# Kernel tuning notes

Measured on AMD Instinct MI355X. Metric: run time of the kernel, lower is better.

Reference implementation:

```python
import jax, jax.numpy as jnp
import numpy as np

B, N, D = 32, 1024, 128


def setup_inputs() -> dict:
    key = jax.random.key(0)
    ks = jax.random.split(key, 8)
    scale = 0.05
    P = jax.random.normal(ks[0], (B, N, D), dtype=jnp.float32)
    w_itr_att = jax.random.normal(ks[1], (3 * D,), dtype=jnp.float32) * scale
    w1 = jax.random.normal(ks[2], (2 * D, D), dtype=jnp.float32) * scale
    w2 = jax.random.normal(ks[3], (2 * D, D), dtype=jnp.float32) * scale
    w3 = jax.random.normal(ks[4], (2 * D, D), dtype=jnp.float32) * scale
    b1 = jnp.zeros((D,), dtype=jnp.float32)
    b2 = jnp.zeros((D,), dtype=jnp.float32)
    b3 = jnp.zeros((D,), dtype=jnp.float32)
    return {"P": P, "w_itr_att": w_itr_att, "w1": w1, "w2": w2,
            "w3": w3, "b1": b1, "b2": b2, "b3": b3}


def reference(P, w_itr_att, w1, w2, w3, b1, b2, b3):
    # P: [b, n, d]
    d = P.shape[-1]
    # Original builds alphaP[b,i,:,j] = concat(P[b,j], P[b,i], P[b,j]*P[b,i])
    # and A[b,i,j] = w_itr_att . alphaP[b,i,:,j]. Decompose w to avoid the
    # O(n^2 * 3d) tensor while computing identical math.
    wa, wb, wc = w_itr_att[:d], w_itr_att[d:2 * d], w_itr_att[2 * d:]
    A = (P @ wb)[:, :, None] + (P @ wa)[:, None, :] \
        + jnp.einsum('bid,bjd->bij', P * wc, P)  # [b, n, n]
    SA = jax.nn.softmax(A, axis=-1)              # softmax over j (axis=2)
    itr_attn = jnp.einsum('bij,bjd->bid', SA, P)  # batch_dot(SA, P)
    # Fuse gate (dropout is identity at inference)
    P_concat = jnp.concatenate([P, itr_attn], axis=2)  # [b, n, 2d]
    z = jnp.tanh(P_concat @ w1 + b1)
    r = jax.nn.sigmoid(P_concat @ w2 + b2)
    f = jax.nn.sigmoid(P_concat @ w3 + b3)
    return r * P + f * z
```

## Files before the change

### kernel.cpp

```cpp
#include <hip/hip_runtime.h>
#include <math.h>

#define BB 32
#define NN 1024
#define DD 128

typedef __bf16 bf16;
typedef bf16 bf16x4 __attribute__((ext_vector_type(4)));
typedef bf16 bf16x8 __attribute__((ext_vector_type(8)));
typedef float f32x4 __attribute__((ext_vector_type(4)));
typedef float f32x16 __attribute__((ext_vector_type(16)));

#define MFMA16(a, b, c) __builtin_amdgcn_mfma_f32_16x16x32_bf16(a, b, c, 0, 0, 0)
#define MFMA32(a, b, c) __builtin_amdgcn_mfma_f32_32x32x16_bf16(a, b, c, 0, 0, 0)

__device__ inline bf16x4 swap32(bf16x4 v) {
    union { bf16x4 h; int i[2]; } u, r;
    u.h = v;
    r.i[0] = __shfl_xor(u.i[0], 32, 64);
    r.i[1] = __shfl_xor(u.i[1], 32, 64);
    return r.h;
}

#define LTS 133
__global__ __launch_bounds__(256) void k_prep(const float* __restrict__ P,
                                              const float* __restrict__ w_itr,
                                              bf16* __restrict__ Xbf,
                                              bf16* __restrict__ Pq,
                                              bf16* __restrict__ Ptp,
                                              float* __restrict__ t) {
    __shared__ float Lt[64 * LTS];
    int tid = threadIdx.x;
    int b = blockIdx.x >> 4, g = blockIdx.x & 15;
    int n0 = g * 64;
    long base = ((long)b * NN + n0) * DD;
#pragma unroll
    for (int i = 0; i < 8; ++i) {
        int idx = tid + i * 256;
        int row = idx >> 5, c4 = idx & 31;
        *(float4*)&Lt[row * LTS + c4 * 4] = *(const float4*)&P[base + row * 128 + c4 * 4];
    }
    __syncthreads();
    {
        int row = tid >> 2, q = tid & 3;
        float s = 0.f;
#pragma unroll
        for (int kk = 0; kk < 32; ++kk) {
            int k = 4 * kk + q;
            s += Lt[row * LTS + k] * w_itr[k];
        }
        s += __shfl_xor(s, 1);
        s += __shfl_xor(s, 2);
        if (q == 0) t[(long)b * NN + n0 + row] = s;
    }
    const float* wc = w_itr + 2 * DD;
#pragma unroll
    for (int i = 0; i < 4; ++i) {
        int idx = tid + i * 256;
        int row = idx >> 4, seg = idx & 15;
        float4 va = *(const float4*)&Lt[row * LTS + seg * 8];
        float4 vb = *(const float4*)&Lt[row * LTS + seg * 8 + 4];
        float4 wa4 = *(const float4*)&wc[seg * 8];
        float4 wb4 = *(const float4*)&wc[seg * 8 + 4];
        float fv[8] = {va.x, va.y, va.z, va.w, vb.x, vb.y, vb.z, vb.w};
        float wv[8] = {wa4.x, wa4.y, wa4.z, wa4.w, wb4.x, wb4.y, wb4.z, wb4.w};
        bf16x8 xv, qv;
#pragma unroll
        for (int e = 0; e < 8; ++e) {
            xv[e] = (bf16)fv[e];
            qv[e] = (bf16)(fv[e] * wv[e]);
        }
        long rowg = (long)b * NN + n0 + row;
        *(bf16x8*)&Xbf[rowg * 128 + seg * 8] = xv;
        *(bf16x8*)&Pq[rowg * 128 + seg * 8] = qv;
    }
#pragma unroll
    for (int i = 0; i < 4; ++i) {
        int idx = tid + i * 256;
        int d = idx >> 3, c = idx & 7;
        bf16x8 v;
#pragma unroll
        for (int e = 0; e < 8; ++e) v[e] = (bf16)Lt[(c * 8 + e) * LTS + d];
        *(bf16x8*)&Ptp[((long)b * DD + d) * NN + n0 + c * 8] = v;
    }
}

__global__ __launch_bounds__(256) void k_prepw(const float* __restrict__ w1,
                                               const float* __restrict__ w2,
                                               const float* __restrict__ w3,
                                               bf16* __restrict__ WtG) {
    __shared__ float Lw[32][33];
    int bi = blockIdx.x;
    int mat = bi >> 5, rem = bi & 31;
    int kt = rem >> 2, ct = rem & 3;
    const float* wsrc = (mat == 0) ? w1 : ((mat == 1) ? w2 : w3);
    int tid = threadIdx.x;
#pragma unroll
    for (int p = 0; p < 4; ++p) {
        int idx = tid + p * 256;
        int kr = idx >> 5, c = idx & 31;
        Lw[kr][c] = wsrc[(kt * 32 + kr) * DD + ct * 32 + c];
    }
    __syncthreads();
    int colg = tid >> 3, kq = tid & 7;
    bf16x4 v;
#pragma unroll
    for (int e = 0; e < 4; ++e) v[e] = (bf16)Lw[kq * 4 + e][colg];
    *(bf16x4*)&WtG[(mat * 128 + ct * 32 + colg) * 256 + kt * 32 + kq * 4] = v;
}

__global__ __launch_bounds__(256, 3) void k_attn(const bf16* __restrict__ Xbf,
                                                 const bf16* __restrict__ Pq,
                                                 const bf16* __restrict__ Ptp,
                                                 const float* __restrict__ t,
                                                 const bf16* __restrict__ WtG,
                                                 const float* __restrict__ b1,
                                                 const float* __restrict__ b2,
                                                 const float* __restrict__ b3,
                                                 float* __restrict__ out) {
    __shared__ __align__(16) char smem[51200];
    float* PA   = (float*)smem;
    bf16*  Wst  = (bf16*)smem;
    float* ost  = (float*)smem;
    bf16*  Xsh  = (bf16*)(smem + 33792);
    float* lbuf = (float*)(smem + 50688);

    const int tid = threadIdx.x;
    const int kh = tid >> 6, lane = tid & 63;
    const int col = lane & 31, q = lane >> 5;
    const int b = blockIdx.x & 31, qt = blockIdx.x >> 5;
    const long qrow0 = (long)b * NN + qt * 32;
    const long kvrow = (long)b * NN;

    bf16x8 Qb[8];
#pragma unroll
    for (int c = 0; c < 8; ++c)
        Qb[c] = *(const bf16x8*)&Pq[(qrow0 + col) * 128 + c * 16 + q * 8];

    f32x16 O[4];
#pragma unroll
    for (int mt = 0; mt < 4; ++mt)
#pragma unroll
        for (int r = 0; r < 16; ++r) O[mt][r] = 0.f;
    float lsum = 0.f;

    for (int kt = 0; kt < 8; ++kt) {
        int j0 = kh * 256 + kt * 32;
        bf16x8 kf[8];
#pragma unroll
        for (int c = 0; c < 8; ++c)
            kf[c] = *(const bf16x8*)&Xbf[(kvrow + j0 + col) * 128 + c * 16 + q * 8];
        bf16x8 vf[4][2];
#pragma unroll
        for (int mt = 0; mt < 4; ++mt)
#pragma unroll
            for (int kc = 0; kc < 2; ++kc)
                vf[mt][kc] = *(const bf16x8*)&Ptp[((long)b * DD + mt * 32 + col) * NN +
                                                  j0 + kc * 16 + q * 8];
        float tqs[16];
#pragma unroll
        for (int i = 0; i < 4; ++i) {
            float4 tv = *(const float4*)&t[kvrow + j0 + 8 * i + 4 * q];
            tqs[4 * i + 0] = tv.x; tqs[4 * i + 1] = tv.y;
            tqs[4 * i + 2] = tv.z; tqs[4 * i + 3] = tv.w;
        }
        f32x16 S;
#pragma unroll
        for (int r = 0; r < 16; ++r) S[r] = 0.f;
#pragma unroll
        for (int c = 0; c < 8; ++c) S = MFMA32(kf[c], Qb[c], S);

        float pv[16];
#pragma unroll
        for (int r = 0; r < 16; ++r) {
            float e = __expf(fminf(S[r] + tqs[r], 80.f));
            pv[r] = e;
            lsum += e;
        }
        bf16x4 Qd[4];
#pragma unroll
        for (int i = 0; i < 4; ++i)
#pragma unroll
            for (int e = 0; e < 4; ++e) Qd[i][e] = (bf16)pv[4 * i + e];
        bf16x4 sA = q ? Qd[0] : Qd[1];
        bf16x4 rA = swap32(sA);
        bf16x4 sB = q ? Qd[2] : Qd[3];
        bf16x4 rB = swap32(sB);
        bf16x4 lo0 = q ? rA : Qd[0], hi0 = q ? Qd[1] : rA;
        bf16x4 lo1 = q ? rB : Qd[2], hi1 = q ? Qd[3] : rB;
        bf16x8 f0, f1;
#pragma unroll
        for (int e = 0; e < 4; ++e) {
            f0[e] = lo0[e]; f0[4 + e] = hi0[e];
            f1[e] = lo1[e]; f1[4 + e] = hi1[e];
        }
#pragma unroll
        for (int mt = 0; mt < 4; ++mt) {
            O[mt] = MFMA32(vf[mt][0], f0, O[mt]);
            O[mt] = MFMA32(vf[mt][1], f1, O[mt]);
        }
    }

    float l2 = lsum + __shfl_xor(lsum, 32, 64);
    if (q == 0) lbuf[kh * 32 + col] = l2;
    if (kh & 1) {
        int slot = kh >> 1;
#pragma unroll
        for (int mt = 0; mt < 4; ++mt)
#pragma unroll
            for (int r = 0; r < 16; ++r) {
                int d = mt * 32 + (r & 3) + 8 * (r >> 2) + 4 * q;
                PA[slot * 4224 + d * 33 + col] = O[mt][r];
            }
    }
    __syncthreads();
    if (!(kh & 1)) {
        int slot = kh >> 1;
#pragma unroll
        for (int mt = 0; mt < 4; ++mt)
#pragma unroll
            for (int r = 0; r < 16; ++r) {
                int d = mt * 32 + (r & 3) + 8 * (r >> 2) + 4 * q;
                O[mt][r] += PA[slot * 4224 + d * 33 + col];
            }
    }
    __syncthreads();
    if (kh == 2) {
#pragma unroll
        for (int mt = 0; mt < 4; ++mt)
#pragma unroll
            for (int r = 0; r < 16; ++r) {
                int d = mt * 32 + (r & 3) + 8 * (r >> 2) + 4 * q;
                PA[d * 33 + col] = O[mt][r];
            }
    } else if (kh & 1) {
        int t128 = (kh >> 1) * 64 + lane;
#pragma unroll
        for (int i = 0; i < 4; ++i) {
            int idx = t128 + i * 128;
            int row = idx >> 4, seg = idx & 15;
            *(bf16x8*)&Xsh[row * 264 + seg * 8] =
                *(const bf16x8*)&Xbf[(qrow0 + row) * 128 + seg * 8];
        }
    }
    __syncthreads();
    if (kh == 0) {
        float ltot = lbuf[col] + lbuf[32 + col] + lbuf[64 + col] + lbuf[96 + col];
        float linv = 1.f / ltot;
#pragma unroll
        for (int mt = 0; mt < 4; ++mt)
#pragma unroll
            for (int r = 0; r < 16; ++r) {
                int d = mt * 32 + (r & 3) + 8 * (r >> 2) + 4 * q;
                float v = (O[mt][r] + PA[d * 33 + col]) * linv;
                Xsh[col * 264 + 128 + d] = (bf16)v;
            }
    }

    const int ln = lane & 15, q3 = lane >> 4;
    const int rh = kh & 1, ch = kh >> 1;
    f32x4 gz[4], gr[4];
    float rres[16];
#pragma unroll
    for (int mat = 0; mat < 3; ++mat) {
        f32x4 acc[4];
#pragma unroll
        for (int nt = 0; nt < 4; ++nt) acc[nt] = (f32x4){0.f, 0.f, 0.f, 0.f};
#pragma unroll
        for (int k2 = 0; k2 < 4; ++k2) {
            __syncthreads();
#pragma unroll
            for (int i = 0; i < 4; ++i) {
                int idx = tid + i * 256;
                *(float4*)&Wst[(idx >> 3) * 72 + (idx & 7) * 8] =
                    *(const float4*)&WtG[(mat * 128 + (idx >> 3)) * 256 + k2 * 64 +
                                         (idx & 7) * 8];
            }
            __syncthreads();
#pragma unroll
            for (int kc2 = 0; kc2 < 2; ++kc2) {
                bf16x8 Af = *(const bf16x8*)&Xsh[(rh * 16 + ln) * 264 + k2 * 64 +
                                                 kc2 * 32 + q3 * 8];
#pragma unroll
                for (int nt = 0; nt < 4; ++nt) {
                    bf16x8 Bf = *(const bf16x8*)&Wst[(ch * 64 + nt * 16 + ln) * 72 +
                                                     kc2 * 32 + q3 * 8];
                    acc[nt] = MFMA16(Af, Bf, acc[nt]);
                }
            }
        }
        const float* bp = (mat == 0) ? b1 : ((mat == 1) ? b2 : b3);
#pragma unroll
        for (int nt = 0; nt < 4; ++nt) {
            int colc = ch * 64 + nt * 16 + ln;
            float bb = bp[colc];
#pragma unroll
            for (int r = 0; r < 4; ++r) {
                float y = acc[nt][r] + bb;
                if (mat == 0) gz[nt][r] = tanhf(y);
                else if (mat == 1) gr[nt][r] = 1.f / (1.f + __expf(-y));
                else {
                    float fg = 1.f / (1.f + __expf(-y));
                    int lrow = rh * 16 + q3 * 4 + r;
                    float p = (float)Xsh[lrow * 264 + colc];
                    rres[nt * 4 + r] = gr[nt][r] * p + fg * gz[nt][r];
                }
            }
        }
    }
    __syncthreads();
#pragma unroll
    for (int nt = 0; nt < 4; ++nt)
#pragma unroll
        for (int r = 0; r < 4; ++r)
            ost[(rh * 16 + q3 * 4 + r) * 132 + ch * 64 + nt * 16 + ln] = rres[nt * 4 + r];
    __syncthreads();
#pragma unroll
    for (int i = 0; i < 4; ++i) {
        int idx = tid + i * 256;
        int row = idx >> 5, c4 = idx & 31;
        float4 v = *(const float4*)&ost[row * 132 + c4 * 4];
        *(float4*)&out[(qrow0 + row) * 128 + c4 * 4] = v;
    }
}

extern "C" void kernel_launch(void* const* d_in, const int* in_sizes, int n_in,
                              void* d_out, int out_size, void* d_ws, size_t ws_size,
                              hipStream_t stream) {
    const float* P     = (const float*)d_in[0];
    const float* w_itr = (const float*)d_in[1];
    const float* w1    = (const float*)d_in[2];
    const float* w2    = (const float*)d_in[3];
    const float* w3    = (const float*)d_in[4];
    const float* b1    = (const float*)d_in[5];
    const float* b2    = (const float*)d_in[6];
    const float* b3    = (const float*)d_in[7];
    float* out = (float*)d_out;

    char* wsb = (char*)d_ws;
    bf16* Xbf  = (bf16*)(wsb);
    bf16* Pq   = (bf16*)(wsb + 8388608);
    bf16* Ptp  = (bf16*)(wsb + 16777216);
    float* tws = (float*)(wsb + 25165824);
    bf16* WtG  = (bf16*)(wsb + 25296896);

    k_prep<<<dim3(BB * 16), dim3(256), 0, stream>>>(P, w_itr, Xbf, Pq, Ptp, tws);
    k_prepw<<<dim3(96), dim3(256), 0, stream>>>(w1, w2, w3, WtG);
    k_attn<<<dim3(1024), dim3(256), 0, stream>>>(Xbf, Pq, Ptp, tws, WtG, b1, b2, b3, out);
}
```

Baseline: 176.6 us.

## Shrink LDS with bf16 partials, raise occupancy, use fast rcp activations, split prep finer

The cross-wave partial output buffers are now stored in bf16 instead of fp32, which cuts k_attn shared memory so the launch bound can target 4 blocks per CU instead of 3. Sigmoid and tanh switch to hardware reciprocal approximations, the softmax exp clamp is removed, and the normalisation uses rcp. k_prep handles 32 rows per block with twice as many blocks. Risks are precision loss from the bf16 partial sums and overflow without the exp clamp, plus register pressure at the higher occupancy.

```diff
diff --git a/kernel.cpp b/kernel.cpp
--- a/kernel.cpp
+++ b/kernel.cpp
@@ -20,6 +20,12 @@
     r.i[0] = __shfl_xor(u.i[0], 32, 64);
     r.i[1] = __shfl_xor(u.i[1], 32, 64);
     return r.h;
+}
+__device__ inline float fsig(float y) {
+    return __builtin_amdgcn_rcpf(1.f + __expf(-y));
+}
+__device__ inline float ftanh(float y) {
+    return 2.f * __builtin_amdgcn_rcpf(1.f + __expf(-2.f * y)) - 1.f;
 }
 
 #define LTS 133
@@ -29,33 +35,31 @@
                                               bf16* __restrict__ Pq,
                                               bf16* __restrict__ Ptp,
                                               float* __restrict__ t) {
-    __shared__ float Lt[64 * LTS];
+    __shared__ float Lt[32 * LTS];
     int tid = threadIdx.x;
-    int b = blockIdx.x >> 4, g = blockIdx.x & 15;
-    int n0 = g * 64;
+    int b = blockIdx.x >> 5, g = blockIdx.x & 31;
+    int n0 = g * 32;
     long base = ((long)b * NN + n0) * DD;
 #pragma unroll
-    for (int i = 0; i < 8; ++i) {
+    for (int i = 0; i < 4; ++i) {
         int idx = tid + i * 256;
         int row = idx >> 5, c4 = idx & 31;
         *(float4*)&Lt[row * LTS + c4 * 4] = *(const float4*)&P[base + row * 128 + c4 * 4];
     }
     __syncthreads();
     {
-        int row = tid >> 2, q = tid & 3;
+        int row = tid >> 3, q = tid & 7;
         float s = 0.f;
 #pragma unroll
-        for (int kk = 0; kk < 32; ++kk) {
-            int k = 4 * kk + q;
-            s += Lt[row * LTS + k] * w_itr[k];
-        }
+        for (int kk = 0; kk < 16; ++kk) s += Lt[row * LTS + kk * 8 + q] * w_itr[kk * 8 + q];
         s += __shfl_xor(s, 1);
         s += __shfl_xor(s, 2);
+        s += __shfl_xor(s, 4);
         if (q == 0) t[(long)b * NN + n0 + row] = s;
     }
     const float* wc = w_itr + 2 * DD;
 #pragma unroll
-    for (int i = 0; i < 4; ++i) {
+    for (int i = 0; i < 2; ++i) {
         int idx = tid + i * 256;
         int row = idx >> 4, seg = idx & 15;
         float4 va = *(const float4*)&Lt[row * LTS + seg * 8];
@@ -75,9 +79,9 @@
         *(bf16x8*)&Pq[rowg * 128 + seg * 8] = qv;
     }
 #pragma unroll
-    for (int i = 0; i < 4; ++i) {
+    for (int i = 0; i < 2; ++i) {
         int idx = tid + i * 256;
-        int d = idx >> 3, c = idx & 7;
+        int d = idx >> 2, c = idx & 3;
         bf16x8 v;
 #pragma unroll
         for (int e = 0; e < 8; ++e) v[e] = (bf16)Lt[(c * 8 + e) * LTS + d];
@@ -109,7 +113,7 @@
     *(bf16x4*)&WtG[(mat * 128 + ct * 32 + colg) * 256 + kt * 32 + kq * 4] = v;
 }
 
-__global__ __launch_bounds__(256, 3) void k_attn(const bf16* __restrict__ Xbf,
+__global__ __launch_bounds__(256, 4) void k_attn(const bf16* __restrict__ Xbf,
                                                  const bf16* __restrict__ Pq,
                                                  const bf16* __restrict__ Ptp,
                                                  const float* __restrict__ t,
@@ -118,12 +122,12 @@
                                                  const float* __restrict__ b2,
                                                  const float* __restrict__ b3,
                                                  float* __restrict__ out) {
-    __shared__ __align__(16) char smem[51200];
-    float* PA   = (float*)smem;
+    __shared__ __align__(16) char smem[35840];
+    bf16*  PA   = (bf16*)smem;
     bf16*  Wst  = (bf16*)smem;
     float* ost  = (float*)smem;
-    bf16*  Xsh  = (bf16*)(smem + 33792);
-    float* lbuf = (float*)(smem + 50688);
+    bf16*  Xsh  = (bf16*)(smem + 18432);
+    float* lbuf = (float*)(smem + 35328);
 
     const int tid = threadIdx.x;
     const int kh = tid >> 6, lane = tid & 63;
@@ -173,7 +177,7 @@
         float pv[16];
 #pragma unroll
         for (int r = 0; r < 16; ++r) {
-            float e = __expf(fminf(S[r] + tqs[r], 80.f));
+            float e = __expf(S[r] + tqs[r]);
             pv[r] = e;
             lsum += e;
         }
@@ -210,7 +214,7 @@
 #pragma unroll
             for (int r = 0; r < 16; ++r) {
                 int d = mt * 32 + (r & 3) + 8 * (r >> 2) + 4 * q;
-                PA[slot * 4224 + d * 33 + col] = O[mt][r];
+                PA[slot * 4608 + d * 36 + col] = (bf16)O[mt][r];
             }
     }
     __syncthreads();
@@ -221,7 +225,7 @@
 #pragma unroll
             for (int r = 0; r < 16; ++r) {
                 int d = mt * 32 + (r & 3) + 8 * (r >> 2) + 4 * q;
-                O[mt][r] += PA[slot * 4224 + d * 33 + col];
+                O[mt][r] += (float)PA[slot * 4608 + d * 36 + col];
             }
     }
     __syncthreads();
@@ -231,7 +235,7 @@
 #pragma unroll
             for (int r = 0; r < 16; ++r) {
                 int d = mt * 32 + (r & 3) + 8 * (r >> 2) + 4 * q;
-                PA[d * 33 + col] = O[mt][r];
+                PA[d * 36 + col] = (bf16)O[mt][r];
             }
     } else if (kh & 1) {
         int t128 = (kh >> 1) * 64 + lane;
@@ -246,13 +250,13 @@
     __syncthreads();
     if (kh == 0) {
         float ltot = lbuf[col] + lbuf[32 + col] + lbuf[64 + col] + lbuf[96 + col];
-        float linv = 1.f / ltot;
+        float linv = __builtin_amdgcn_rcpf(ltot);
 #pragma unroll
         for (int mt = 0; mt < 4; ++mt)
 #pragma unroll
             for (int r = 0; r < 16; ++r) {
                 int d = mt * 32 + (r & 3) + 8 * (r >> 2) + 4 * q;
-                float v = (O[mt][r] + PA[d * 33 + col]) * linv;
+                float v = (O[mt][r] + (float)PA[d * 36 + col]) * linv;
                 Xsh[col * 264 + 128 + d] = (bf16)v;
             }
     }
@@ -297,10 +301,10 @@
 #pragma unroll
             for (int r = 0; r < 4; ++r) {
                 float y = acc[nt][r] + bb;
-                if (mat == 0) gz[nt][r] = tanhf(y);
-                else if (mat == 1) gr[nt][r] = 1.f / (1.f + __expf(-y));
+                if (mat == 0) gz[nt][r] = ftanh(y);
+                else if (mat == 1) gr[nt][r] = fsig(y);
                 else {
-                    float fg = 1.f / (1.f + __expf(-y));
+                    float fg = fsig(y);
                     int lrow = rh * 16 + q3 * 4 + r;
                     float p = (float)Xsh[lrow * 264 + colc];
                     rres[nt * 4 + r] = gr[nt][r] * p + fg * gz[nt][r];
@@ -344,7 +348,7 @@
     float* tws = (float*)(wsb + 25165824);
     bf16* WtG  = (bf16*)(wsb + 25296896);
 
-    k_prep<<<dim3(BB * 16), dim3(256), 0, stream>>>(P, w_itr, Xbf, Pq, Ptp, tws);
+    k_prep<<<dim3(BB * 32), dim3(256), 0, stream>>>(P, w_itr, Xbf, Pq, Ptp, tws);
     k_prepw<<<dim3(96), dim3(256), 0, stream>>>(w1, w2, w3, WtG);
     k_attn<<<dim3(1024), dim3(256), 0, stream>>>(Xbf, Pq, Ptp, tws, WtG, b1, b2, b3, out);
 }
```

New measurement: 286.9 us. +62.5%, slower.
